# Performance work log

Hardware: AMD Instinct MI355X
Metric: run time of the kernel (lower is better)

Reference implementation:

```python
import jax, jax.numpy as jnp
import numpy as np

B, S = 128, 200
Q, K, V, C, SUM = 20000, 128, 128, 64, 128


def setup_inputs() -> dict:
    key = jax.random.key(0)
    ks = jax.random.split(key, 14)
    stdev = 1.0 / np.sqrt(C + K)  # NTM-style memory init bound

    def lin_w(k, fan_in, shape):
        b = 1.0 / np.sqrt(fan_in)
        return jax.random.uniform(k, shape, jnp.float32, -b, b)

    # embeddings with padding_idx=0 zeroed (PAD_INDEX=0)
    q_emb = jax.random.normal(ks[0], (Q + 1, K), jnp.float32).at[0].set(0.0)
    i_emb = jax.random.normal(ks[1], (2 * Q + 1, V), jnp.float32).at[0].set(0.0)
    key_memory = jax.random.uniform(ks[2], (K, C), jnp.float32, -stdev, stdev)
    init_value_memory = jax.random.uniform(ks[3], (V, C), jnp.float32, -stdev, stdev)
    erase_W = lin_w(ks[4], V, (V, V))
    erase_b = lin_w(ks[5], V, (V,))
    add_W = lin_w(ks[6], V, (V, V))
    add_b = lin_w(ks[7], V, (V,))
    summ_W = lin_w(ks[8], V + K, (V + K, SUM))
    summ_b = lin_w(ks[9], V + K, (SUM,))
    out_W = lin_w(ks[10], SUM, (SUM, 1))
    out_b = lin_w(ks[11], SUM, (1,))
    inp = jax.random.randint(ks[12], (B, S), 0, 2 * Q + 1)
    target_id = jax.random.randint(ks[13], (B,), 0, Q + 1)
    return dict(q_emb=q_emb, i_emb=i_emb, key_memory=key_memory,
                init_value_memory=init_value_memory,
                erase_W=erase_W, erase_b=erase_b, add_W=add_W, add_b=add_b,
                summ_W=summ_W, summ_b=summ_b, out_W=out_W, out_b=out_b,
                input=inp, target_id=target_id)


def reference(q_emb, i_emb, key_memory, init_value_memory,
              erase_W, erase_b, add_W, add_b,
              summ_W, summ_b, out_W, out_b,
              input, target_id):
    Qn = q_emb.shape[0] - 1
    bsz = input.shape[0]
    # map interaction index -> question id
    qid = input - Qn * (input > Qn).astype(input.dtype)          # (B,S)
    # all per-step quantities are independent of memory state -> precompute
    iv = i_emb[input]                                            # (B,S,V)
    e = jax.nn.sigmoid(iv @ erase_W + erase_b)                   # (B,S,V)
    a = jnp.tanh(iv @ add_W + add_b)                             # (B,S,V)
    w = jax.nn.softmax(q_emb[qid] @ key_memory, axis=-1)         # (B,S,C)

    mem0 = jnp.broadcast_to(init_value_memory, (bsz,) + init_value_memory.shape)  # (B,V,C)

    def step(mem, xs):
        e_t, a_t, w_t = xs                                       # (B,V),(B,V),(B,C)
        erase = e_t[:, :, None] * w_t[:, None, :]                # rank-1 outer, (B,V,C)
        add = a_t[:, :, None] * w_t[:, None, :]
        mem = mem * (1.0 - erase) + add
        return mem, None

    xs = (jnp.swapaxes(e, 0, 1), jnp.swapaxes(a, 0, 1), jnp.swapaxes(w, 0, 1))
    mem, _ = jax.lax.scan(step, mem0, xs)                        # (B,V,C)

    qv = q_emb[target_id]                                        # (B,K)
    wt = jax.nn.softmax(qv @ key_memory, axis=-1)                # (B,C)
    read = jnp.einsum('bvc,bc->bv', mem, wt)                     # (B,V)
    summ = jnp.tanh(jnp.concatenate([read, qv], axis=-1) @ summ_W + summ_b)
    return summ @ out_W + out_b                                  # (B,1), pre-sigmoid
```

## Files before the change

### kernel.cpp

```cpp
#include <hip/hip_runtime.h>
#include <hip/hip_bf16.h>
#include <hip/hip_fp16.h>

#define B_ 128
#define S_ 200
#define QN_ 20000
#define V_ 128
#define K_ 128
#define C_ 64
#define SUM_ 128
#define NCH 4
#define CL 50
#define RP 52

using short8 = __attribute__((ext_vector_type(8))) short;
using f32x4  = __attribute__((ext_vector_type(4))) float;

__device__ __forceinline__ float fast_sigmoid(float x) { return 1.f / (1.f + __expf(-x)); }
__device__ __forceinline__ float fast_tanh(float x)    { return 1.f - 2.f / (__expf(2.f * x) + 1.f); }

template<bool BF>
__device__ __forceinline__ float ld(const void* p, long long i) {
    if (BF) return __bfloat162float(((const __hip_bfloat16*)p)[i]);
    return ((const float*)p)[i];
}

__device__ __forceinline__ unsigned short f2bf(float v) {
    __hip_bfloat16 h = __float2bfloat16(v);
    unsigned short u;
    __builtin_memcpy(&u, &h, 2);
    return u;
}

__device__ __forceinline__ int probe_flag_wave(const void* erase_b) {
    const unsigned* w = (const unsigned*)erase_b;
    const int lane = threadIdx.x & 63;
    const unsigned lo = w[lane] & 0xffffu;
    const float f = __uint_as_float(lo << 16);
    const unsigned long long bal = __ballot(!(fabsf(f) <= 0.5f));
    return (__popcll(bal) <= 8) ? 1 : 0;
}

struct FusedLDS {
    unsigned short ivA[RP * 136];
    unsigned short qvA[RP * 136];
    __half esh[RP * 136];
    __half ash[RP * 136];
    float  wlog[RP * 68];
    int sidx[RP], sqid[RP];
};

template<bool BF>
__device__ __forceinline__ void fused_body(
    const void* q_emb, const void* i_emb,
    const void* erase_W, const void* add_W, const void* key_memory,
    const void* erase_b, const void* add_b,
    const int* __restrict__ input,
    __half* __restrict__ du, FusedLDS& sm)
{
    const int bid = blockIdx.x;
    const int b = bid & 127;
    const int chunk = bid >> 7;
    const int t = threadIdx.x;
    const int wv = t >> 6;
    const int lane = t & 63;
    const int lrow = lane & 15;
    const int lk8 = (lane >> 4) * 8;

    if (t < RP) {
        const int s = (t < CL) ? t : 0;
        const int ix = input[b * S_ + chunk * CL + s];
        sm.sidx[t] = ix;
        sm.sqid[t] = ix > QN_ ? ix - QN_ : ix;
    }
    __syncthreads();

    #pragma unroll
    for (int r = 0; r < 7; ++r) {
        const int j = t + 256 * r;
        if (j < 2 * RP * 16) {
            const int tensor = j >= RP * 16;
            const int jj = j - tensor * (RP * 16);
            const int row = jj >> 4;
            const int seg = jj & 15;
            const int gr = tensor ? sm.sqid[row] : sm.sidx[row];
            unsigned short* dst = (tensor ? sm.qvA : sm.ivA) + row * 136 + seg * 8;
            if (BF) {
                const unsigned short* src = (const unsigned short*)(tensor ? q_emb : i_emb);
                *(uint4*)dst = *(const uint4*)(src + (long long)gr * 128 + seg * 8);
            } else {
                const float* src = (const float*)(tensor ? q_emb : i_emb) + (long long)gr * 128 + seg * 8;
                const float4 f0 = *(const float4*)src;
                const float4 f1 = *(const float4*)(src + 4);
                unsigned short o[8] = {f2bf(f0.x), f2bf(f0.y), f2bf(f0.z), f2bf(f0.w),
                                       f2bf(f1.x), f2bf(f1.y), f2bf(f1.z), f2bf(f1.w)};
                *(uint4*)dst = *(const uint4*)o;
            }
        }
    }

    short8 bfr[5][4];
    int nco[5];
    float biasq[4];
    #pragma unroll
    for (int q = 0; q < 5; ++q) {
        const int nt = wv + 4 * q;
        const void* Wsrc;
        int ldn;
        if (q < 2)      { Wsrc = erase_W;    nco[q] = nt * 16 + lrow;        ldn = 128; }
        else if (q < 4) { Wsrc = add_W;      nco[q] = (nt - 8) * 16 + lrow;  ldn = 128; }
        else            { Wsrc = key_memory; nco[q] = (nt - 16) * 16 + lrow; ldn = 64; }
        if (q < 2)      biasq[q] = ld<BF>(erase_b, nco[q]);
        else if (q < 4) biasq[q] = ld<BF>(add_b, nco[q]);
        #pragma unroll
        for (int ks = 0; ks < 4; ++ks) {
            unsigned short o[8];
            #pragma unroll
            for (int jj = 0; jj < 8; ++jj) {
                const long long idx = (long long)(ks * 32 + lk8 + jj) * ldn + nco[q];
                o[jj] = f2bf(ld<BF>(Wsrc, idx));
            }
            bfr[q][ks] = *(const short8*)o;
        }
    }
    __syncthreads();

    #pragma unroll
    for (int mt = 0; mt < 4; ++mt) {
        short8 afr[4];
        const unsigned short* ar = sm.ivA + (mt * 16 + lrow) * 136 + lk8;
        #pragma unroll
        for (int ks = 0; ks < 4; ++ks)
            afr[ks] = *(const short8*)(ar + ks * 32);
        #pragma unroll
        for (int q = 0; q < 4; ++q) {
            f32x4 acc = {0.f, 0.f, 0.f, 0.f};
            #pragma unroll
            for (int ks = 0; ks < 4; ++ks)
                acc = __builtin_amdgcn_mfma_f32_16x16x32_bf16(afr[ks], bfr[q][ks], acc, 0, 0, 0);
            const int ncol = nco[q];
            const float bb = biasq[q];
            #pragma unroll
            for (int r = 0; r < 4; ++r) {
                const int orow = mt * 16 + (lane >> 4) * 4 + r;
                if (orow < CL) {
                    const float y = acc[r] + bb;
                    if (q < 2) sm.esh[orow * 136 + ncol] = __float2half(fast_sigmoid(y));
                    else       sm.ash[orow * 136 + ncol] = __float2half(fast_tanh(y));
                }
            }
        }
    }
    #pragma unroll
    for (int mt = 0; mt < 4; ++mt) {
        short8 afr[4];
        const unsigned short* ar = sm.qvA + (mt * 16 + lrow) * 136 + lk8;
        #pragma unroll
        for (int ks = 0; ks < 4; ++ks)
            afr[ks] = *(const short8*)(ar + ks * 32);
        f32x4 acc = {0.f, 0.f, 0.f, 0.f};
        #pragma unroll
        for (int ks = 0; ks < 4; ++ks)
            acc = __builtin_amdgcn_mfma_f32_16x16x32_bf16(afr[ks], bfr[4][ks], acc, 0, 0, 0);
        #pragma unroll
        for (int r = 0; r < 4; ++r) {
            const int orow = mt * 16 + (lane >> 4) * 4 + r;
            if (orow < CL)
                sm.wlog[orow * 68 + nco[4]] = acc[r];
        }
    }
    __syncthreads();

    #pragma unroll
    for (int pass = 0; pass < 2; ++pass) {
        const int row = pass * 32 + (t >> 3);
        if (row < CL) {
            const int cs = t & 7;
            float* wr = &sm.wlog[row * 68 + cs * 8];
            float v[8];
            *(float4*)&v[0] = *(const float4*)&wr[0];
            *(float4*)&v[4] = *(const float4*)&wr[4];
            float m = v[0];
            #pragma unroll
            for (int ii = 1; ii < 8; ++ii) m = fmaxf(m, v[ii]);
            m = fmaxf(m, __shfl_xor(m, 1, 64));
            m = fmaxf(m, __shfl_xor(m, 2, 64));
            m = fmaxf(m, __shfl_xor(m, 4, 64));
            float s = 0.f;
            #pragma unroll
            for (int ii = 0; ii < 8; ++ii) { v[ii] = __expf(v[ii] - m); s += v[ii]; }
            s += __shfl_xor(s, 1, 64);
            s += __shfl_xor(s, 2, 64);
            s += __shfl_xor(s, 4, 64);
            const float inv = 1.f / s;
            *(float4*)&wr[0] = make_float4(v[0]*inv, v[1]*inv, v[2]*inv, v[3]*inv);
            *(float4*)&wr[4] = make_float4(v[4]*inv, v[5]*inv, v[6]*inv, v[7]*inv);
        }
    }
    __syncthreads();

    const int vg = t >> 3;
    const int cg = t & 7;
    const int v0 = vg * 4, c0 = cg * 8;

    const __half2 one2 = __floats2half2_rn(1.f, 1.f);
    const __half2 zero2 = __floats2half2_rn(0.f, 0.f);
    __half2 Dm2[4][4], Um2[4][4];
    #pragma unroll
    for (int i = 0; i < 4; ++i)
        #pragma unroll
        for (int jp = 0; jp < 4; ++jp) { Dm2[i][jp] = one2; Um2[i][jp] = zero2; }

    for (int s = 0; s < CL; ++s) {
        const __half2 e01 = *(const __half2*)(sm.esh + s * 136 + v0);
        const __half2 e23 = *(const __half2*)(sm.esh + s * 136 + v0 + 2);
        const __half2 a01 = *(const __half2*)(sm.ash + s * 136 + v0);
        const __half2 a23 = *(const __half2*)(sm.ash + s * 136 + v0 + 2);
        const float4 wf0 = *(const float4*)(sm.wlog + s * 68 + c0);
        const float4 wf1 = *(const float4*)(sm.wlog + s * 68 + c0 + 4);
        const __half2 w2[4] = { __floats2half2_rn(wf0.x, wf0.y), __floats2half2_rn(wf0.z, wf0.w),
                                __floats2half2_rn(wf1.x, wf1.y), __floats2half2_rn(wf1.z, wf1.w) };
        const __half2 e2[4] = { __low2half2(e01), __high2half2(e01),
                                __low2half2(e23), __high2half2(e23) };
        const __half2 a2[4] = { __low2half2(a01), __high2half2(a01),
                                __low2half2(a23), __high2half2(a23) };
        #pragma unroll
        for (int i = 0; i < 4; ++i) {
            const __half2 ne = __hneg2(e2[i]);
            #pragma unroll
            for (int jp = 0; jp < 4; ++jp) {
                const __half2 d2 = __hfma2(ne, w2[jp], one2);
                Dm2[i][jp] = __hmul2(Dm2[i][jp], d2);
                Um2[i][jp] = __hfma2(d2, Um2[i][jp], __hmul2(a2[i], w2[jp]));
            }
        }
    }

    __half* dbase = du + ((size_t)(chunk * B_ + b) * (V_ * C_ * 2));
    #pragma unroll
    for (int i = 0; i < 4; ++i) {
        __half* dst = dbase + (size_t)(v0 + i) * (C_ * 2) + c0;
        *(uint4*)dst        = *(const uint4*)&Dm2[i][0];
        *(uint4*)(dst + C_) = *(const uint4*)&Um2[i][0];
    }
}

__global__ __launch_bounds__(256) void dkvmn_fused(
    const void* q_emb, const void* i_emb,
    const void* erase_W, const void* add_W, const void* key_memory,
    const void* erase_b, const void* add_b,
    const int* __restrict__ input,
    __half* __restrict__ du)
{
    __shared__ FusedLDS sm;
    if (probe_flag_wave(erase_b))
        fused_body<true>(q_emb, i_emb, erase_W, add_W, key_memory,
                         erase_b, add_b, input, du, sm);
    else
        fused_body<false>(q_emb, i_emb, erase_W, add_W, key_memory,
                          erase_b, add_b, input, du, sm);
}

template<bool BF>
__device__ __forceinline__ void foldfinal_body(
    const void* init_value_memory, const void* q_emb, const void* key_memory,
    const void* summ_W, const void* summ_b,
    const void* out_W, const void* out_b,
    const int* __restrict__ target_id,
    const __half* __restrict__ du,
    void* __restrict__ outp, float* wtl, float* readl, float* summl)
{
    const int b = blockIdx.x;
    const int t = threadIdx.x;
    const int cg = t & 7;
    const int c0 = cg * 8;

    if (t < 64) {
        const long long qrow = (long long)target_id[b] * K_;
        float logit = 0.f;
        #pragma unroll 8
        for (int i = 0; i < K_; ++i)
            logit += ld<BF>(q_emb, qrow + i) * ld<BF>(key_memory, i * C_ + t);
        float m = logit;
        for (int off = 32; off > 0; off >>= 1)
            m = fmaxf(m, __shfl_xor(m, off, 64));
        const float ex = __expf(logit - m);
        float ssum = ex;
        for (int off = 32; off > 0; off >>= 1)
            ssum += __shfl_xor(ssum, off, 64);
        wtl[t] = ex / ssum;
    }
    __syncthreads();

    float wt8[8];
    *(float4*)&wt8[0] = *(const float4*)(wtl + c0);
    *(float4*)&wt8[4] = *(const float4*)(wtl + c0 + 4);

    #pragma unroll
    for (int sub = 0; sub < 4; ++sub) {
        const int v = sub * 32 + (t >> 3);

        uint4 qa[NCH], qb[NCH];
        #pragma unroll
        for (int ch = 0; ch < NCH; ++ch) {
            const __half* base = du + ((size_t)(ch * B_ + b) * (V_ * C_ * 2))
                                    + (size_t)v * (C_ * 2) + c0;
            qa[ch] = *(const uint4*)base;
            qb[ch] = *(const uint4*)(base + C_);
        }

        float mem[8];
        #pragma unroll
        for (int k = 0; k < 8; ++k)
            mem[k] = ld<BF>(init_value_memory, v * C_ + c0 + k);

        #pragma unroll
        for (int ch = 0; ch < NCH; ++ch) {
            const __half2* hD = (const __half2*)&qa[ch];
            const __half2* hU = (const __half2*)&qb[ch];
            #pragma unroll
            for (int k = 0; k < 4; ++k) {
                const float2 fD = __half22float2(hD[k]);
                const float2 fU = __half22float2(hU[k]);
                mem[2 * k]     = fmaf(fD.x, mem[2 * k],     fU.x);
                mem[2 * k + 1] = fmaf(fD.y, mem[2 * k + 1], fU.y);
            }
        }

        float pacc = 0.f;
        #pragma unroll
        for (int k = 0; k < 8; ++k) pacc += mem[k] * wt8[k];
        pacc += __shfl_xor(pacc, 1, 64);
        pacc += __shfl_xor(pacc, 2, 64);
        pacc += __shfl_xor(pacc, 4, 64);
        if (cg == 0) readl[v] = pacc;
    }
    __syncthreads();

    if (t < SUM_) {
        const long long qrow = (long long)target_id[b] * K_;
        float acc = ld<BF>(summ_b, t);
        #pragma unroll 8
        for (int i = 0; i < 128; ++i)
            acc += readl[i] * ld<BF>(summ_W, i * SUM_ + t);
        #pragma unroll 8
        for (int i = 0; i < 128; ++i)
            acc += ld<BF>(q_emb, qrow + i) * ld<BF>(summ_W, (128 + i) * SUM_ + t);
        summl[t] = fast_tanh(acc);
    }
    __syncthreads();

    if (t < 64) {
        float oacc = summl[t] * ld<BF>(out_W, t) + summl[t + 64] * ld<BF>(out_W, t + 64);
        for (int off = 32; off > 0; off >>= 1)
            oacc += __shfl_xor(oacc, off, 64);
        if (t == 0) {
            const float res = oacc + ld<BF>(out_b, 0);
            if (BF) ((__hip_bfloat16*)outp)[b] = __float2bfloat16(res);
            else    ((float*)outp)[b] = res;
        }
    }
}

__global__ __launch_bounds__(256) void dkvmn_foldfinal(
    const void* init_value_memory, const void* q_emb, const void* key_memory,
    const void* summ_W, const void* summ_b,
    const void* out_W, const void* out_b, const void* erase_b,
    const int* __restrict__ target_id,
    const __half* __restrict__ du,
    void* __restrict__ outp)
{
    __shared__ float wtl[C_], readl[V_], summl[SUM_];
    if (probe_flag_wave(erase_b))
        foldfinal_body<true>(init_value_memory, q_emb, key_memory, summ_W, summ_b,
                             out_W, out_b, target_id, du, outp, wtl, readl, summl);
    else
        foldfinal_body<false>(init_value_memory, q_emb, key_memory, summ_W, summ_b,
                              out_W, out_b, target_id, du, outp, wtl, readl, summl);
}

extern "C" void kernel_launch(void* const* d_in, const int* in_sizes, int n_in,
                              void* d_out, int out_size, void* d_ws, size_t ws_size,
                              hipStream_t stream) {
    const void* q_emb             = d_in[0];
    const void* i_emb             = d_in[1];
    const void* key_memory        = d_in[2];
    const void* init_value_memory = d_in[3];
    const void* erase_W           = d_in[4];
    const void* erase_b           = d_in[5];
    const void* add_W             = d_in[6];
    const void* add_b             = d_in[7];
    const void* summ_W            = d_in[8];
    const void* summ_b            = d_in[9];
    const void* out_W             = d_in[10];
    const void* out_b             = d_in[11];
    const int* input     = (const int*)d_in[12];
    const int* target_id = (const int*)d_in[13];

    __half* du = (__half*)d_ws;

    dkvmn_fused<<<NCH * B_, 256, 0, stream>>>(
        q_emb, i_emb, erase_W, add_W, key_memory, erase_b, add_b, input, du);
    dkvmn_foldfinal<<<B_, 256, 0, stream>>>(
        init_value_memory, q_emb, key_memory, summ_W, summ_b, out_W, out_b,
        erase_b, target_id, du, d_out);
}
```

Measured before the change: 140.9 us.

## Split sequence into eight chunks and alias LDS buffers for e/a outputs

Doubles the number of time chunks per batch row from four to eight, with 25 steps each, so twice as many blocks run the fused projection and chunked scan and each block's serial recurrence is half as long. The gathered embedding tiles now share LDS with the sigmoid/tanh outputs: fragments are loaded into registers, a barrier is taken, and the results are written into the same buffers. This cuts LDS per block, which may allow more blocks per CU. In exchange, MFMA padding waste rises (32 rows computed for 25 used), and the combine stage has more chunk partials to merge.

```diff
diff --git a/kernel.cpp b/kernel.cpp
--- a/kernel.cpp
+++ b/kernel.cpp
@@ -9,9 +9,9 @@
 #define K_ 128
 #define C_ 64
 #define SUM_ 128
-#define NCH 4
-#define CL 50
-#define RP 52
+#define NCH 8
+#define CL 25
+#define RW 32
 
 using short8 = __attribute__((ext_vector_type(8))) short;
 using f32x4  = __attribute__((ext_vector_type(4))) float;
@@ -42,12 +42,10 @@
 }
 
 struct FusedLDS {
-    unsigned short ivA[RP * 136];
-    unsigned short qvA[RP * 136];
-    __half esh[RP * 136];
-    __half ash[RP * 136];
-    float  wlog[RP * 68];
-    int sidx[RP], sqid[RP];
+    unsigned short bufA[RW * 136];
+    unsigned short bufB[RW * 136];
+    float  wlog[RW * 68];
+    int sidx[RW], sqid[RW];
 };
 
 template<bool BF>
@@ -67,7 +65,7 @@
     const int lrow = lane & 15;
     const int lk8 = (lane >> 4) * 8;
 
-    if (t < RP) {
+    if (t < RW) {
         const int s = (t < CL) ? t : 0;
         const int ix = input[b * S_ + chunk * CL + s];
         sm.sidx[t] = ix;
@@ -76,26 +74,23 @@
     __syncthreads();
 
     #pragma unroll
-    for (int r = 0; r < 7; ++r) {
+    for (int r = 0; r < 4; ++r) {
         const int j = t + 256 * r;
-        if (j < 2 * RP * 16) {
-            const int tensor = j >= RP * 16;
-            const int jj = j - tensor * (RP * 16);
-            const int row = jj >> 4;
-            const int seg = jj & 15;
-            const int gr = tensor ? sm.sqid[row] : sm.sidx[row];
-            unsigned short* dst = (tensor ? sm.qvA : sm.ivA) + row * 136 + seg * 8;
-            if (BF) {
-                const unsigned short* src = (const unsigned short*)(tensor ? q_emb : i_emb);
-                *(uint4*)dst = *(const uint4*)(src + (long long)gr * 128 + seg * 8);
-            } else {
-                const float* src = (const float*)(tensor ? q_emb : i_emb) + (long long)gr * 128 + seg * 8;
-                const float4 f0 = *(const float4*)src;
-                const float4 f1 = *(const float4*)(src + 4);
-                unsigned short o[8] = {f2bf(f0.x), f2bf(f0.y), f2bf(f0.z), f2bf(f0.w),
-                                       f2bf(f1.x), f2bf(f1.y), f2bf(f1.z), f2bf(f1.w)};
-                *(uint4*)dst = *(const uint4*)o;
-            }
+        const int tensor = j >> 9;
+        const int row = (j >> 4) & 31;
+        const int seg = j & 15;
+        const int gr = tensor ? sm.sqid[row] : sm.sidx[row];
+        unsigned short* dst = (tensor ? sm.bufB : sm.bufA) + row * 136 + seg * 8;
+        if (BF) {
+            const unsigned short* src = (const unsigned short*)(tensor ? q_emb : i_emb);
+            *(uint4*)dst = *(const uint4*)(src + (long long)gr * 128 + seg * 8);
+        } else {
+            const float* src = (const float*)(tensor ? q_emb : i_emb) + (long long)gr * 128 + seg * 8;
+            const float4 f0 = *(const float4*)src;
+            const float4 f1 = *(const float4*)(src + 4);
+            unsigned short o[8] = {f2bf(f0.x), f2bf(f0.y), f2bf(f0.z), f2bf(f0.w),
+                                   f2bf(f1.x), f2bf(f1.y), f2bf(f1.z), f2bf(f1.w)};
+            *(uint4*)dst = *(const uint4*)o;
         }
     }
 
@@ -125,83 +120,77 @@
     }
     __syncthreads();
 
-    #pragma unroll
-    for (int mt = 0; mt < 4; ++mt) {
-        short8 afr[4];
-        const unsigned short* ar = sm.ivA + (mt * 16 + lrow) * 136 + lk8;
-        #pragma unroll
-        for (int ks = 0; ks < 4; ++ks)
-            afr[ks] = *(const short8*)(ar + ks * 32);
+    __half* eshw = (__half*)sm.bufA;
+    __half* ashw = (__half*)sm.bufB;
+    #pragma unroll
+    for (int mt = 0; mt < 2; ++mt) {
+        short8 afr_iv[4], afr_qv[4];
+        const unsigned short* arA = sm.bufA + (mt * 16 + lrow) * 136 + lk8;
+        const unsigned short* arB = sm.bufB + (mt * 16 + lrow) * 136 + lk8;
+        #pragma unroll
+        for (int ks = 0; ks < 4; ++ks) {
+            afr_iv[ks] = *(const short8*)(arA + ks * 32);
+            afr_qv[ks] = *(const short8*)(arB + ks * 32);
+        }
+        __syncthreads();
         #pragma unroll
         for (int q = 0; q < 4; ++q) {
             f32x4 acc = {0.f, 0.f, 0.f, 0.f};
             #pragma unroll
             for (int ks = 0; ks < 4; ++ks)
-                acc = __builtin_amdgcn_mfma_f32_16x16x32_bf16(afr[ks], bfr[q][ks], acc, 0, 0, 0);
+                acc = __builtin_amdgcn_mfma_f32_16x16x32_bf16(afr_iv[ks], bfr[q][ks], acc, 0, 0, 0);
             const int ncol = nco[q];
             const float bb = biasq[q];
             #pragma unroll
             for (int r = 0; r < 4; ++r) {
                 const int orow = mt * 16 + (lane >> 4) * 4 + r;
-                if (orow < CL) {
-                    const float y = acc[r] + bb;
-                    if (q < 2) sm.esh[orow * 136 + ncol] = __float2half(fast_sigmoid(y));
-                    else       sm.ash[orow * 136 + ncol] = __float2half(fast_tanh(y));
-                }
+                const float y = acc[r] + bb;
+                if (q < 2) eshw[orow * 136 + ncol] = __float2half(fast_sigmoid(y));
+                else       ashw[orow * 136 + ncol] = __float2half(fast_tanh(y));
             }
         }
-    }
-    #pragma unroll
-    for (int mt = 0; mt < 4; ++mt) {
-        short8 afr[4];
-        const unsigned short* ar = sm.qvA + (mt * 16 + lrow) * 136 + lk8;
-        #pragma unroll
-        for (int ks = 0; ks < 4; ++ks)
-            afr[ks] = *(const short8*)(ar + ks * 32);
-        f32x4 acc = {0.f, 0.f, 0.f, 0.f};
-        #pragma unroll
-        for (int ks = 0; ks < 4; ++ks)
-            acc = __builtin_amdgcn_mfma_f32_16x16x32_bf16(afr[ks], bfr[4][ks], acc, 0, 0, 0);
-        #pragma unroll
-        for (int r = 0; r < 4; ++r) {
-            const int orow = mt * 16 + (lane >> 4) * 4 + r;
-            if (orow < CL)
-                sm.wlog[orow * 68 + nco[4]] = acc[r];
-        }
-    }
-    __syncthreads();
-
-    #pragma unroll
-    for (int pass = 0; pass < 2; ++pass) {
-        const int row = pass * 32 + (t >> 3);
-        if (row < CL) {
-            const int cs = t & 7;
-            float* wr = &sm.wlog[row * 68 + cs * 8];
-            float v[8];
-            *(float4*)&v[0] = *(const float4*)&wr[0];
-            *(float4*)&v[4] = *(const float4*)&wr[4];
-            float m = v[0];
-            #pragma unroll
-            for (int ii = 1; ii < 8; ++ii) m = fmaxf(m, v[ii]);
-            m = fmaxf(m, __shfl_xor(m, 1, 64));
-            m = fmaxf(m, __shfl_xor(m, 2, 64));
-            m = fmaxf(m, __shfl_xor(m, 4, 64));
-            float s = 0.f;
-            #pragma unroll
-            for (int ii = 0; ii < 8; ++ii) { v[ii] = __expf(v[ii] - m); s += v[ii]; }
-            s += __shfl_xor(s, 1, 64);
-            s += __shfl_xor(s, 2, 64);
-            s += __shfl_xor(s, 4, 64);
-            const float inv = 1.f / s;
-            *(float4*)&wr[0] = make_float4(v[0]*inv, v[1]*inv, v[2]*inv, v[3]*inv);
-            *(float4*)&wr[4] = make_float4(v[4]*inv, v[5]*inv, v[6]*inv, v[7]*inv);
-        }
+        {
+            f32x4 acc = {0.f, 0.f, 0.f, 0.f};
+            #pragma unroll
+            for (int ks = 0; ks < 4; ++ks)
+                acc = __builtin_amdgcn_mfma_f32_16x16x32_bf16(afr_qv[ks], bfr[4][ks], acc, 0, 0, 0);
+            #pragma unroll
+            for (int r = 0; r < 4; ++r)
+                sm.wlog[(mt * 16 + (lane >> 4) * 4 + r) * 68 + nco[4]] = acc[r];
+        }
+    }
+    __syncthreads();
+
+    {
+        const int row = t >> 3;
+        const int cs = t & 7;
+        float* wr = &sm.wlog[row * 68 + cs * 8];
+        float v[8];
+        *(float4*)&v[0] = *(const float4*)&wr[0];
+        *(float4*)&v[4] = *(const float4*)&wr[4];
+        float m = v[0];
+        #pragma unroll
+        for (int ii = 1; ii < 8; ++ii) m = fmaxf(m, v[ii]);
+        m = fmaxf(m, __shfl_xor(m, 1, 64));
+        m = fmaxf(m, __shfl_xor(m, 2, 64));
+        m = fmaxf(m, __shfl_xor(m, 4, 64));
+        float s = 0.f;
+        #pragma unroll
+        for (int ii = 0; ii < 8; ++ii) { v[ii] = __expf(v[ii] - m); s += v[ii]; }
+        s += __shfl_xor(s, 1, 64);
+        s += __shfl_xor(s, 2, 64);
+        s += __shfl_xor(s, 4, 64);
+        const float inv = 1.f / s;
+        *(float4*)&wr[0] = make_float4(v[0]*inv, v[1]*inv, v[2]*inv, v[3]*inv);
+        *(float4*)&wr[4] = make_float4(v[4]*inv, v[5]*inv, v[6]*inv, v[7]*inv);
     }
     __syncthreads();
 
     const int vg = t >> 3;
     const int cg = t & 7;
     const int v0 = vg * 4, c0 = cg * 8;
+    const __half* esh = (const __half*)sm.bufA;
+    const __half* ash = (const __half*)sm.bufB;
 
     const __half2 one2 = __floats2half2_rn(1.f, 1.f);
     const __half2 zero2 = __floats2half2_rn(0.f, 0.f);
@@ -212,10 +201,10 @@
         for (int jp = 0; jp < 4; ++jp) { Dm2[i][jp] = one2; Um2[i][jp] = zero2; }
 
     for (int s = 0; s < CL; ++s) {
-        const __half2 e01 = *(const __half2*)(sm.esh + s * 136 + v0);
-        const __half2 e23 = *(const __half2*)(sm.esh + s * 136 + v0 + 2);
-        const __half2 a01 = *(const __half2*)(sm.ash + s * 136 + v0);
-        const __half2 a23 = *(const __half2*)(sm.ash + s * 136 + v0 + 2);
+        const __half2 e01 = *(const __half2*)(esh + s * 136 + v0);
+        const __half2 e23 = *(const __half2*)(esh + s * 136 + v0 + 2);
+        const __half2 a01 = *(const __half2*)(ash + s * 136 + v0);
+        const __half2 a23 = *(const __half2*)(ash + s * 136 + v0 + 2);
         const float4 wf0 = *(const float4*)(sm.wlog + s * 68 + c0);
         const float4 wf1 = *(const float4*)(sm.wlog + s * 68 + c0 + 4);
         const __half2 w2[4] = { __floats2half2_rn(wf0.x, wf0.y), __floats2half2_rn(wf0.z, wf0.w),
```

Measured after the change: 166.4 us. +18.0%, slower.
